# Optimization experiments

Hardware: AMD Instinct MI355X
Metric: run time of the kernel (lower is better)

The kernel has to match this reference:

```python
import jax, jax.numpy as jnp
import numpy as np

N, E, D_IN, D_H, D_OUT = 8000, 256000, 128, 128, 64
TEMP = 10.0       # config temperature.value (non-learnable)
WEIGHT = 1.0      # config weight.value (non-learnable)
LN_EPS = 1e-5


def _gcn_conv(x, W, b, src, dst, n):
    # PyG GCNConv: add self loops, sym-normalized aggregation, then bias.
    h = x @ W
    loop = jnp.arange(n)
    s = jnp.concatenate([src, loop])
    d = jnp.concatenate([dst, loop])
    deg = jnp.zeros((n,), h.dtype).at[d].add(1.0)
    dinv = jax.lax.rsqrt(jnp.maximum(deg, 1e-12))
    norm = dinv[s] * dinv[d]                       # [E+N]
    out = jax.ops.segment_sum(h[s] * norm[:, None], d, num_segments=n)
    return out + b


def _entropy_gradient(x, A, temperature, normalize):
    # E_i = 0.5 * sum_j A_ij ||x_i - x_j||^2  (dense adjacency, as in repo)
    sq = jnp.sum(x * x, axis=1)                    # [N]
    Ax = A @ x                                     # [N,d]
    deg = A.sum(axis=1)                            # [N]
    En = 0.5 * (deg * sq + A @ sq - 2.0 * jnp.sum(x * Ax, axis=1))
    if normalize:
        En = En / (jnp.max(En) + 1e-12)
    logits = -En / temperature
    P = jax.nn.softmax(logits)
    logP = jax.nn.log_softmax(logits)
    S = -jnp.sum(P * logP)
    c = P * (logP + S) / temperature               # dS/dE_k
    # dS/dx_i = c_i*(deg_i x_i - (Ax)_i) + (A^T c)_i x_i - (A^T (c*x))_i
    ATc = A.T @ c
    return (c[:, None] * (deg[:, None] * x - Ax)
            + ATc[:, None] * x - A.T @ (c[:, None] * x))


def _layer_norm(x, gamma, beta):
    mu = jnp.mean(x, axis=-1, keepdims=True)
    var = jnp.mean(jnp.square(x - mu), axis=-1, keepdims=True)
    return (x - mu) * jax.lax.rsqrt(var + LN_EPS) * gamma + beta


def setup_inputs() -> dict:
    key = jax.random.key(0)
    ks = jax.random.split(key, 6)
    def w(k, i, o):
        return jax.random.normal(k, (i, o), jnp.float32) / np.sqrt(i).astype(np.float32)
    return {
        "x": jax.random.normal(ks[0], (N, D_IN), jnp.float32),
        "edge_index": jax.random.randint(ks[1], (2, E), 0, N),
        "W1": w(ks[2], D_IN, D_H), "b1": jnp.zeros((D_H,), jnp.float32),
        "W2": w(ks[3], D_H, D_H), "b2": jnp.zeros((D_H,), jnp.float32),
        "W_out": w(ks[4], D_H, D_OUT), "b_out": jnp.zeros((D_OUT,), jnp.float32),
        "ln_gamma": jnp.ones((D_H,), jnp.float32),
        "ln_beta": jnp.zeros((D_H,), jnp.float32),
    }


def reference(x, edge_index, W1, b1, W2, b2, W_out, b_out, ln_gamma, ln_beta):
    n = x.shape[0]
    src, dst = edge_index[0], edge_index[1]
    # dense adjacency (to_dense_adj sums duplicate edges)
    A = jnp.zeros((n, n), x.dtype).at[src, dst].add(1.0)
    for W, b in ((W1, b1), (W2, b2)):
        h = _gcn_conv(x, W, b, src, dst, n)
        eg = jax.lax.stop_gradient(_entropy_gradient(h, A, TEMP, True))
        h = h + WEIGHT * eg
        h = jax.nn.relu(h)
        x = _layer_norm(h, ln_gamma, ln_beta)
    embedding = _gcn_conv(x, W_out, b_out, src, dst, n)
    return embedding
```

## Files before the change

### kernel.cpp

```cpp
#include <hip/hip_runtime.h>
#include <hip/hip_bf16.h>

#define DH 128

static constexpr float TEMP_ = 10.0f;
static constexpr float LN_EPS_ = 1e-5f;

__device__ __forceinline__ float bf2f(unsigned short u) {
  union { unsigned int i; float f; } v; v.i = ((unsigned int)u) << 16; return v.f;
}
__device__ __forceinline__ unsigned short f2bf(float f) {
  union { float f; unsigned int i; } v; v.f = f;
  unsigned int b = v.i + 0x7FFFu + ((v.i >> 16) & 1u);
  return (unsigned short)(b >> 16);
}
__device__ __forceinline__ float4 us4f4(ushort4 u) {
  return make_float4(bf2f(u.x), bf2f(u.y), bf2f(u.z), bf2f(u.w));
}
__device__ __forceinline__ ushort4 f4us4(float4 f) {
  ushort4 u; u.x = f2bf(f.x); u.y = f2bf(f.y); u.z = f2bf(f.z); u.w = f2bf(f.w);
  return u;
}

__device__ __forceinline__ float4 f4_fma(float a, float4 x, float4 y) {
  y.x = fmaf(a, x.x, y.x); y.y = fmaf(a, x.y, y.y);
  y.z = fmaf(a, x.z, y.z); y.w = fmaf(a, x.w, y.w);
  return y;
}
__device__ __forceinline__ float4 f4_add(float4 a, float4 b) {
  a.x += b.x; a.y += b.y; a.z += b.z; a.w += b.w; return a;
}
__device__ __forceinline__ float f4_hsum(float4 a) { return (a.x + a.y) + (a.z + a.w); }

__device__ __forceinline__ float grp_sum32(float v) {
  #pragma unroll
  for (int o = 16; o > 0; o >>= 1) v += __shfl_down(v, o, 32);
  return __shfl(v, 0, 32);
}

__global__ void k_hist(const int* __restrict__ ei, int E, int* cnt_d, int* cnt_s) {
  int e = blockIdx.x * blockDim.x + threadIdx.x;
  if (e < E) {
    atomicAdd(&cnt_s[ei[e]], 1);
    atomicAdd(&cnt_d[ei[E + e]], 1);
  }
}

__global__ __launch_bounds__(1024) void k_scan(int* cnt_d, int* cnt_s,
                                               int* off_d, int* off_s,
                                               float* dinv, float* dego, int n) {
  __shared__ int sm[1024];
  const int t = threadIdx.x;
  const int pass = blockIdx.x;
  int* cnt = pass ? cnt_s : cnt_d;
  int* off = pass ? off_s : off_d;
  const int base = t * 8;
  int lc[8]; int s = 0;
  #pragma unroll
  for (int j = 0; j < 8; ++j) {
    int idx = base + j;
    int v = (idx < n) ? cnt[idx] : 0;
    lc[j] = v; s += v;
  }
  sm[t] = s; __syncthreads();
  for (int o = 1; o < 1024; o <<= 1) {
    int v = (t >= o) ? sm[t - o] : 0;
    __syncthreads();
    sm[t] += v;
    __syncthreads();
  }
  int run = sm[t] - s;
  int total = sm[1023];
  #pragma unroll
  for (int j = 0; j < 8; ++j) {
    int idx = base + j;
    if (idx < n) {
      off[idx] = run; run += lc[j];
      if (pass == 0) dinv[idx] = rsqrtf((float)lc[j] + 1.0f);
      else           dego[idx] = (float)lc[j];
      cnt[idx] = 0;
    }
  }
  if (t == 0) off[n] = total;
}

__global__ void k_fill(const int* __restrict__ ei, int E,
                       const int* __restrict__ off_d, const int* __restrict__ off_s,
                       int* cnt_d, int* cnt_s, int* idx_d, int* idx_s) {
  int e = blockIdx.x * blockDim.x + threadIdx.x;
  if (e < E) {
    int s = ei[e], d = ei[E + e];
    int p = atomicAdd(&cnt_d[d], 1);
    idx_d[off_d[d] + p] = s;
    int q = atomicAdd(&cnt_s[s], 1);
    idx_s[off_s[s] + q] = d;
  }
}

template <int DOUT>
__global__ __launch_bounds__(256) void k_gemm(const float* __restrict__ X,
                                              const float* __restrict__ W,
                                              unsigned short* __restrict__ Hb) {
  __shared__ float Ws[64 * DOUT];
  __shared__ float xs[16 * 128];
  const int t = threadIdx.x;
  const int row0 = blockIdx.x * 16;

  const float4* xg = (const float4*)(X + row0 * 128);
  float4* xs4 = (float4*)xs;
  xs4[t] = xg[t];
  xs4[t + 256] = xg[t + 256];

  constexpr int RPT = (16 * DOUT) / 256;
  const int c = t % DOUT;
  const int rg = t / DOUT;
  float acc[RPT];
  #pragma unroll
  for (int r = 0; r < RPT; ++r) acc[r] = 0.f;

  for (int kt = 0; kt < 2; ++kt) {
    __syncthreads();
    for (int i = t; i < 64 * DOUT; i += 256) Ws[i] = W[kt * 64 * DOUT + i];
    __syncthreads();
    for (int k = 0; k < 64; ++k) {
      float wv = Ws[k * DOUT + c];
      #pragma unroll
      for (int r = 0; r < RPT; ++r)
        acc[r] += xs[(rg * RPT + r) * 128 + kt * 64 + k] * wv;
    }
  }
  #pragma unroll
  for (int r = 0; r < RPT; ++r)
    Hb[(row0 + rg * RPT + r) * DOUT + c] = f2bf(acc[r]);
}

__global__ __launch_bounds__(256) void k_conv_agg(const unsigned short* __restrict__ Hb,
                                                  const float* __restrict__ dinv,
                                                  const float* __restrict__ b,
                                                  const int* __restrict__ off_d,
                                                  const int* __restrict__ idx_d,
                                                  float* __restrict__ G,
                                                  unsigned short* __restrict__ Gb,
                                                  float* __restrict__ sq) {
  const int lane = threadIdx.x & 31;
  const int i = blockIdx.x * 8 + (threadIdx.x >> 5);
  const ushort4* Hv = (const ushort4*)Hb;
  const float di = dinv[i];
  float4 acc = us4f4(Hv[i * 32 + lane]);
  acc.x *= di; acc.y *= di; acc.z *= di; acc.w *= di;
  int o = off_d[i];
  const int oe = off_d[i + 1];
  for (; o + 4 <= oe; o += 4) {
    int s0 = idx_d[o], s1 = idx_d[o + 1], s2 = idx_d[o + 2], s3 = idx_d[o + 3];
    ushort4 r0 = Hv[s0 * 32 + lane], r1 = Hv[s1 * 32 + lane];
    ushort4 r2 = Hv[s2 * 32 + lane], r3 = Hv[s3 * 32 + lane];
    float d0 = dinv[s0], d1 = dinv[s1], d2 = dinv[s2], d3 = dinv[s3];
    acc = f4_fma(d0, us4f4(r0), acc); acc = f4_fma(d1, us4f4(r1), acc);
    acc = f4_fma(d2, us4f4(r2), acc); acc = f4_fma(d3, us4f4(r3), acc);
  }
  for (; o < oe; ++o) {
    int s = idx_d[o];
    acc = f4_fma(dinv[s], us4f4(Hv[s * 32 + lane]), acc);
  }
  float4 bb = ((const float4*)b)[lane];
  float4 gi;
  gi.x = fmaf(di, acc.x, bb.x); gi.y = fmaf(di, acc.y, bb.y);
  gi.z = fmaf(di, acc.z, bb.z); gi.w = fmaf(di, acc.w, bb.w);
  ((float4*)G)[i * 32 + lane] = gi;
  ((ushort4*)Gb)[i * 32 + lane] = f4us4(gi);
  float s2 = grp_sum32(gi.x * gi.x + gi.y * gi.y + gi.z * gi.z + gi.w * gi.w);
  if (lane == 0) sq[i] = s2;
}

__global__ __launch_bounds__(256) void k_ax_en(const float* __restrict__ G,
                                               const unsigned short* __restrict__ Gb,
                                               const float* __restrict__ sq,
                                               const float* __restrict__ dego,
                                               const int* __restrict__ off_s,
                                               const int* __restrict__ idx_s,
                                               float* __restrict__ Ax,
                                               float* __restrict__ En) {
  const int lane = threadIdx.x & 31;
  const int i = blockIdx.x * 8 + (threadIdx.x >> 5);
  const ushort4* Gv = (const ushort4*)Gb;
  float4 axf = make_float4(0.f, 0.f, 0.f, 0.f);
  float asq = 0.f;
  int o = off_s[i];
  const int oe = off_s[i + 1];
  for (; o + 4 <= oe; o += 4) {
    int d0 = idx_s[o], d1 = idx_s[o + 1], d2 = idx_s[o + 2], d3 = idx_s[o + 3];
    ushort4 r0 = Gv[d0 * 32 + lane], r1 = Gv[d1 * 32 + lane];
    ushort4 r2 = Gv[d2 * 32 + lane], r3 = Gv[d3 * 32 + lane];
    asq += (sq[d0] + sq[d1]) + (sq[d2] + sq[d3]);
    axf = f4_add(axf, f4_add(f4_add(us4f4(r0), us4f4(r1)),
                             f4_add(us4f4(r2), us4f4(r3))));
  }
  for (; o < oe; ++o) {
    int d = idx_s[o];
    axf = f4_add(axf, us4f4(Gv[d * 32 + lane]));
    asq += sq[d];
  }
  ((float4*)Ax)[i * 32 + lane] = axf;
  float4 gi = ((const float4*)G)[i * 32 + lane];
  float dot = grp_sum32(gi.x * axf.x + gi.y * axf.y + gi.z * axf.z + gi.w * axf.w);
  if (lane == 0) En[i] = 0.5f * (dego[i] * sq[i] + asq - 2.f * dot);
}

__device__ __forceinline__ float red1024(float v, bool domax, float* sm) {
  #pragma unroll
  for (int o = 32; o > 0; o >>= 1) {
    float u = __shfl_down(v, o, 64);
    v = domax ? fmaxf(v, u) : v + u;
  }
  if ((threadIdx.x & 63) == 0) sm[threadIdx.x >> 6] = v;
  __syncthreads();
  if (threadIdx.x == 0) {
    float r = sm[0];
    for (int k = 1; k < 16; ++k) r = domax ? fmaxf(r, sm[k]) : r + sm[k];
    sm[0] = r;
  }
  __syncthreads();
  float r = sm[0];
  __syncthreads();
  return r;
}

__global__ __launch_bounds__(1024) void k_softc(const float* __restrict__ En,
                                                float* __restrict__ c, int n) {
  __shared__ float sm[16];
  const int t = threadIdx.x;
  float m = -1e30f;
  for (int i = t; i < n; i += 1024) m = fmaxf(m, En[i]);
  m = red1024(m, true, sm);
  const float denom = (m + 1e-12f) * TEMP_;
  float se = 0.f;
  for (int i = t; i < n; i += 1024) se += expf(-En[i] / denom);
  se = red1024(se, false, sm);
  const float logZ = logf(se);
  float Sacc = 0.f;
  for (int i = t; i < n; i += 1024) {
    float li = -En[i] / denom;
    float P = expf(li) / se;
    Sacc -= P * (li - logZ);
  }
  float S = red1024(Sacc, false, sm);
  for (int i = t; i < n; i += 1024) {
    float li = -En[i] / denom;
    float P = expf(li) / se;
    c[i] = P * ((li - logZ) + S) / TEMP_;
  }
}

__global__ __launch_bounds__(256) void k_combine_ln(const float* __restrict__ G,
                                                    const unsigned short* __restrict__ Gb,
                                                    const float* __restrict__ Ax,
                                                    const float* __restrict__ cvec,
                                                    const float* __restrict__ dego,
                                                    const int* __restrict__ off_d,
                                                    const int* __restrict__ idx_d,
                                                    const float* __restrict__ gamma,
                                                    const float* __restrict__ beta,
                                                    float* __restrict__ Xout) {
  const int lane = threadIdx.x & 31;
  const int i = blockIdx.x * 8 + (threadIdx.x >> 5);
  const ushort4* Gv = (const ushort4*)Gb;
  const float4 gi = ((const float4*)G)[i * 32 + lane];
  float4 tf = make_float4(0.f, 0.f, 0.f, 0.f);
  float atc = 0.f;
  int o = off_d[i];
  const int oe = off_d[i + 1];
  for (; o + 4 <= oe; o += 4) {
    int s0 = idx_d[o], s1 = idx_d[o + 1], s2 = idx_d[o + 2], s3 = idx_d[o + 3];
    ushort4 r0 = Gv[s0 * 32 + lane], r1 = Gv[s1 * 32 + lane];
    ushort4 r2 = Gv[s2 * 32 + lane], r3 = Gv[s3 * 32 + lane];
    float c0 = cvec[s0], c1 = cvec[s1], c2 = cvec[s2], c3 = cvec[s3];
    atc += (c0 + c1) + (c2 + c3);
    tf = f4_fma(c0, us4f4(r0), tf); tf = f4_fma(c1, us4f4(r1), tf);
    tf = f4_fma(c2, us4f4(r2), tf); tf = f4_fma(c3, us4f4(r3), tf);
  }
  for (; o < oe; ++o) {
    int s = idx_d[o];
    float cs = cvec[s];
    atc += cs;
    tf = f4_fma(cs, us4f4(Gv[s * 32 + lane]), tf);
  }
  const float ci = cvec[i], dg = dego[i];
  const float4 axi = ((const float4*)Ax)[i * 32 + lane];
  float4 v;
  v.x = fmaxf(gi.x + ci * (dg * gi.x - axi.x) + atc * gi.x - tf.x, 0.f);
  v.y = fmaxf(gi.y + ci * (dg * gi.y - axi.y) + atc * gi.y - tf.y, 0.f);
  v.z = fmaxf(gi.z + ci * (dg * gi.z - axi.z) + atc * gi.z - tf.z, 0.f);
  v.w = fmaxf(gi.w + ci * (dg * gi.w - axi.w) + atc * gi.w - tf.w, 0.f);
  float mu = grp_sum32(f4_hsum(v)) * (1.f / 128.f);
  float4 dv;
  dv.x = v.x - mu; dv.y = v.y - mu; dv.z = v.z - mu; dv.w = v.w - mu;
  float var = grp_sum32(dv.x * dv.x + dv.y * dv.y + dv.z * dv.z + dv.w * dv.w) * (1.f / 128.f);
  float rs = rsqrtf(var + LN_EPS_);
  float4 ga = ((const float4*)gamma)[lane];
  float4 be = ((const float4*)beta)[lane];
  float4 out;
  out.x = fmaf(dv.x * rs, ga.x, be.x);
  out.y = fmaf(dv.y * rs, ga.y, be.y);
  out.z = fmaf(dv.z * rs, ga.z, be.z);
  out.w = fmaf(dv.w * rs, ga.w, be.w);
  ((float4*)Xout)[i * 32 + lane] = out;
}

__global__ __launch_bounds__(256) void k_final_agg(const unsigned short* __restrict__ Hb,
                                                   const float* __restrict__ dinv,
                                                   const float* __restrict__ bout,
                                                   const int* __restrict__ off_d,
                                                   const int* __restrict__ idx_d,
                                                   float* __restrict__ out) {
  const int lane = threadIdx.x & 15;
  const int i = blockIdx.x * 16 + (threadIdx.x >> 4);
  const ushort4* Hv = (const ushort4*)Hb;
  const float di = dinv[i];
  float4 acc = us4f4(Hv[i * 16 + lane]);
  acc.x *= di; acc.y *= di; acc.z *= di; acc.w *= di;
  int o = off_d[i];
  const int oe = off_d[i + 1];
  for (; o + 4 <= oe; o += 4) {
    int s0 = idx_d[o], s1 = idx_d[o + 1], s2 = idx_d[o + 2], s3 = idx_d[o + 3];
    ushort4 r0 = Hv[s0 * 16 + lane], r1 = Hv[s1 * 16 + lane];
    ushort4 r2 = Hv[s2 * 16 + lane], r3 = Hv[s3 * 16 + lane];
    acc = f4_fma(dinv[s0], us4f4(r0), acc); acc = f4_fma(dinv[s1], us4f4(r1), acc);
    acc = f4_fma(dinv[s2], us4f4(r2), acc); acc = f4_fma(dinv[s3], us4f4(r3), acc);
  }
  for (; o < oe; ++o) {
    int s = idx_d[o];
    acc = f4_fma(dinv[s], us4f4(Hv[s * 16 + lane]), acc);
  }
  float4 bb = ((const float4*)bout)[lane];
  float4 r;
  r.x = fmaf(di, acc.x, bb.x); r.y = fmaf(di, acc.y, bb.y);
  r.z = fmaf(di, acc.z, bb.z); r.w = fmaf(di, acc.w, bb.w);
  ((float4*)out)[i * 16 + lane] = r;
}

extern "C" void kernel_launch(void* const* d_in, const int* in_sizes, int n_in,
                              void* d_out, int out_size, void* d_ws, size_t ws_size,
                              hipStream_t stream) {
  const float* x    = (const float*)d_in[0];
  const int*   ei   = (const int*)d_in[1];
  const float* W1   = (const float*)d_in[2];
  const float* b1   = (const float*)d_in[3];
  const float* W2   = (const float*)d_in[4];
  const float* b2   = (const float*)d_in[5];
  const float* Wout = (const float*)d_in[6];
  const float* bout = (const float*)d_in[7];
  const float* gam  = (const float*)d_in[8];
  const float* bet  = (const float*)d_in[9];
  float* out = (float*)d_out;

  const int N = in_sizes[0] / DH;
  const int E = in_sizes[1] / 2;

  float* ws = (float*)d_ws;
  float* xf = ws;   ws += N * DH;
  float* G  = ws;   ws += N * DH;
  float* Ax = ws;   ws += N * DH;
  float* sq = ws;   ws += N;
  float* En = ws;   ws += N;
  float* cv = ws;   ws += N;
  float* dinv = ws; ws += N;
  float* dego = ws; ws += N;
  unsigned short* Hb = (unsigned short*)ws; ws += N * DH / 2;
  unsigned short* Gb = (unsigned short*)ws; ws += N * DH / 2;
  int* cnt_d = (int*)ws; ws += N;
  int* cnt_s = (int*)ws; ws += N;
  int* off_d = (int*)ws; ws += N + 4;
  int* off_s = (int*)ws; ws += N + 4;
  int* idx_d = (int*)ws; ws += E;
  int* idx_s = (int*)ws; ws += E;

  hipMemsetAsync(cnt_d, 0, 2 * N * sizeof(int), stream);
  k_hist<<<(E + 255) / 256, 256, 0, stream>>>(ei, E, cnt_d, cnt_s);
  k_scan<<<2, 1024, 0, stream>>>(cnt_d, cnt_s, off_d, off_s, dinv, dego, N);
  k_fill<<<(E + 255) / 256, 256, 0, stream>>>(ei, E, off_d, off_s, cnt_d, cnt_s,
                                              idx_d, idx_s);

  const float* xin = x;
  const float* Wl[2] = {W1, W2};
  const float* bl[2] = {b1, b2};
  for (int l = 0; l < 2; ++l) {
    k_gemm<DH><<<N / 16, 256, 0, stream>>>(xin, Wl[l], Hb);
    k_conv_agg<<<N / 8, 256, 0, stream>>>(Hb, dinv, bl[l], off_d, idx_d, G, Gb, sq);
    k_ax_en<<<N / 8, 256, 0, stream>>>(G, Gb, sq, dego, off_s, idx_s, Ax, En);
    k_softc<<<1, 1024, 0, stream>>>(En, cv, N);
    k_combine_ln<<<N / 8, 256, 0, stream>>>(G, Gb, Ax, cv, dego, off_d, idx_d,
                                            gam, bet, xf);
    xin = xf;
  }
  k_gemm<64><<<N / 16, 256, 0, stream>>>(xf, Wout, Hb);
  k_final_agg<<<N / 16, 256, 0, stream>>>(Hb, dinv, bout, off_d, idx_d, out);
}
```

Before: 277.3 us.

## Fuse softmax-entropy coefficients into combine kernel and merge histogram with first GEMM

Removes the single-block softmax/entropy kernel. Each combine_ln block now redundantly reduces the max and the exp-sums over all N energies, then recomputes the coefficient c per neighbor from En inline. The edge histogram is also folded into the first layer's GEMM launch as extra blocks, saving a launch and overlapping the atomics with the matmul. In exchange, every one of the 1000 blocks rereads the full En array and runs two block reductions, plus extra exp work per edge, and fast __expf/__logf replace the precise versions.

Measured after the change: 271.2 us. 2.2% less time.

```diff
diff --git a/kernel.cpp b/kernel.cpp
--- a/kernel.cpp
+++ b/kernel.cpp
@@ -38,12 +38,98 @@
   return __shfl(v, 0, 32);
 }
 
-__global__ void k_hist(const int* __restrict__ ei, int E, int* cnt_d, int* cnt_s) {
-  int e = blockIdx.x * blockDim.x + threadIdx.x;
-  if (e < E) {
-    atomicAdd(&cnt_s[ei[e]], 1);
-    atomicAdd(&cnt_d[ei[E + e]], 1);
-  }
+__device__ __forceinline__ float blkred(float v, bool mx, float* s4) {
+  const int t = threadIdx.x;
+  #pragma unroll
+  for (int o = 32; o > 0; o >>= 1) {
+    float u = __shfl_down(v, o, 64);
+    v = mx ? fmaxf(v, u) : v + u;
+  }
+  __syncthreads();
+  if ((t & 63) == 0) s4[t >> 6] = v;
+  __syncthreads();
+  float r = mx ? fmaxf(fmaxf(s4[0], s4[1]), fmaxf(s4[2], s4[3]))
+               : (s4[0] + s4[1]) + (s4[2] + s4[3]);
+  __syncthreads();
+  return r;
+}
+
+__global__ __launch_bounds__(256) void k_gemm1_hist(const float* __restrict__ X,
+                                                    const float* __restrict__ W,
+                                                    unsigned short* __restrict__ Hb,
+                                                    const int* __restrict__ ei, int E,
+                                                    int* cnt_d, int* cnt_s, int NT) {
+  __shared__ float Ws[64 * DH];
+  __shared__ float xs[16 * 128];
+  const int t = threadIdx.x;
+  if ((int)blockIdx.x < NT) {
+    const int row0 = blockIdx.x * 16;
+    const float4* xg = (const float4*)(X + row0 * 128);
+    float4* xs4 = (float4*)xs;
+    xs4[t] = xg[t];
+    xs4[t + 256] = xg[t + 256];
+    const int c = t & 127, rg = t >> 7;
+    float acc[8];
+    #pragma unroll
+    for (int r = 0; r < 8; ++r) acc[r] = 0.f;
+    for (int kt = 0; kt < 2; ++kt) {
+      __syncthreads();
+      for (int i = t; i < 64 * DH; i += 256) Ws[i] = W[kt * 64 * DH + i];
+      __syncthreads();
+      for (int k = 0; k < 64; ++k) {
+        float wv = Ws[k * DH + c];
+        #pragma unroll
+        for (int r = 0; r < 8; ++r)
+          acc[r] += xs[(rg * 8 + r) * 128 + kt * 64 + k] * wv;
+      }
+    }
+    #pragma unroll
+    for (int r = 0; r < 8; ++r)
+      Hb[(row0 + rg * 8 + r) * DH + c] = f2bf(acc[r]);
+  } else {
+    const int nb = gridDim.x - NT;
+    for (int e = (blockIdx.x - NT) * 256 + t; e < E; e += nb * 256) {
+      atomicAdd(&cnt_s[ei[e]], 1);
+      atomicAdd(&cnt_d[ei[E + e]], 1);
+    }
+  }
+}
+
+template <int DOUT>
+__global__ __launch_bounds__(256) void k_gemm(const float* __restrict__ X,
+                                              const float* __restrict__ W,
+                                              unsigned short* __restrict__ Hb) {
+  __shared__ float Ws[64 * DOUT];
+  __shared__ float xs[16 * 128];
+  const int t = threadIdx.x;
+  const int row0 = blockIdx.x * 16;
+
+  const float4* xg = (const float4*)(X + row0 * 128);
+  float4* xs4 = (float4*)xs;
+  xs4[t] = xg[t];
+  xs4[t + 256] = xg[t + 256];
+
+  constexpr int RPT = (16 * DOUT) / 256;
+  const int c = t % DOUT;
+  const int rg = t / DOUT;
+  float acc[RPT];
+  #pragma unroll
+  for (int r = 0; r < RPT; ++r) acc[r] = 0.f;
+
+  for (int kt = 0; kt < 2; ++kt) {
+    __syncthreads();
+    for (int i = t; i < 64 * DOUT; i += 256) Ws[i] = W[kt * 64 * DOUT + i];
+    __syncthreads();
+    for (int k = 0; k < 64; ++k) {
+      float wv = Ws[k * DOUT + c];
+      #pragma unroll
+      for (int r = 0; r < RPT; ++r)
+        acc[r] += xs[(rg * RPT + r) * 128 + kt * 64 + k] * wv;
+    }
+  }
+  #pragma unroll
+  for (int r = 0; r < RPT; ++r)
+    Hb[(row0 + rg * RPT + r) * DOUT + c] = f2bf(acc[r]);
 }
 
 __global__ __launch_bounds__(1024) void k_scan(int* cnt_d, int* cnt_s,
@@ -95,43 +181,6 @@
     int q = atomicAdd(&cnt_s[s], 1);
     idx_s[off_s[s] + q] = d;
   }
-}
-
-template <int DOUT>
-__global__ __launch_bounds__(256) void k_gemm(const float* __restrict__ X,
-                                              const float* __restrict__ W,
-                                              unsigned short* __restrict__ Hb) {
-  __shared__ float Ws[64 * DOUT];
-  __shared__ float xs[16 * 128];
-  const int t = threadIdx.x;
-  const int row0 = blockIdx.x * 16;
-
-  const float4* xg = (const float4*)(X + row0 * 128);
-  float4* xs4 = (float4*)xs;
-  xs4[t] = xg[t];
-  xs4[t + 256] = xg[t + 256];
-
-  constexpr int RPT = (16 * DOUT) / 256;
-  const int c = t % DOUT;
-  const int rg = t / DOUT;
-  float acc[RPT];
-  #pragma unroll
-  for (int r = 0; r < RPT; ++r) acc[r] = 0.f;
-
-  for (int kt = 0; kt < 2; ++kt) {
-    __syncthreads();
-    for (int i = t; i < 64 * DOUT; i += 256) Ws[i] = W[kt * 64 * DOUT + i];
-    __syncthreads();
-    for (int k = 0; k < 64; ++k) {
-      float wv = Ws[k * DOUT + c];
-      #pragma unroll
-      for (int r = 0; r < RPT; ++r)
-        acc[r] += xs[(rg * RPT + r) * 128 + kt * 64 + k] * wv;
-    }
-  }
-  #pragma unroll
-  for (int r = 0; r < RPT; ++r)
-    Hb[(row0 + rg * RPT + r) * DOUT + c] = f2bf(acc[r]);
 }
 
 __global__ __launch_bounds__(256) void k_conv_agg(const unsigned short* __restrict__ Hb,
@@ -206,63 +255,37 @@
   if (lane == 0) En[i] = 0.5f * (dego[i] * sq[i] + asq - 2.f * dot);
 }
 
-__device__ __forceinline__ float red1024(float v, bool domax, float* sm) {
-  #pragma unroll
-  for (int o = 32; o > 0; o >>= 1) {
-    float u = __shfl_down(v, o, 64);
-    v = domax ? fmaxf(v, u) : v + u;
-  }
-  if ((threadIdx.x & 63) == 0) sm[threadIdx.x >> 6] = v;
-  __syncthreads();
-  if (threadIdx.x == 0) {
-    float r = sm[0];
-    for (int k = 1; k < 16; ++k) r = domax ? fmaxf(r, sm[k]) : r + sm[k];
-    sm[0] = r;
-  }
-  __syncthreads();
-  float r = sm[0];
-  __syncthreads();
-  return r;
-}
-
-__global__ __launch_bounds__(1024) void k_softc(const float* __restrict__ En,
-                                                float* __restrict__ c, int n) {
-  __shared__ float sm[16];
-  const int t = threadIdx.x;
-  float m = -1e30f;
-  for (int i = t; i < n; i += 1024) m = fmaxf(m, En[i]);
-  m = red1024(m, true, sm);
-  const float denom = (m + 1e-12f) * TEMP_;
-  float se = 0.f;
-  for (int i = t; i < n; i += 1024) se += expf(-En[i] / denom);
-  se = red1024(se, false, sm);
-  const float logZ = logf(se);
-  float Sacc = 0.f;
-  for (int i = t; i < n; i += 1024) {
-    float li = -En[i] / denom;
-    float P = expf(li) / se;
-    Sacc -= P * (li - logZ);
-  }
-  float S = red1024(Sacc, false, sm);
-  for (int i = t; i < n; i += 1024) {
-    float li = -En[i] / denom;
-    float P = expf(li) / se;
-    c[i] = P * ((li - logZ) + S) / TEMP_;
-  }
-}
-
 __global__ __launch_bounds__(256) void k_combine_ln(const float* __restrict__ G,
                                                     const unsigned short* __restrict__ Gb,
                                                     const float* __restrict__ Ax,
-                                                    const float* __restrict__ cvec,
+                                                    const float* __restrict__ En,
                                                     const float* __restrict__ dego,
                                                     const int* __restrict__ off_d,
                                                     const int* __restrict__ idx_d,
                                                     const float* __restrict__ gamma,
                                                     const float* __restrict__ beta,
-                                                    float* __restrict__ Xout) {
-  const int lane = threadIdx.x & 31;
-  const int i = blockIdx.x * 8 + (threadIdx.x >> 5);
+                                                    float* __restrict__ Xout, int n) {
+  __shared__ float s4[4];
+  const int t = threadIdx.x;
+  float mloc = -3.0e38f;
+  for (int k = t; k < n; k += 256) mloc = fmaxf(mloc, En[k]);
+  const float m = blkred(mloc, true, s4);
+  const float invden = -1.0f / ((m + 1e-12f) * TEMP_);
+  float se = 0.f, sl = 0.f;
+  for (int k = t; k < n; k += 256) {
+    float li = En[k] * invden;
+    float e = __expf(li);
+    se += e; sl += e * li;
+  }
+  se = blkred(se, false, s4);
+  sl = blkred(sl, false, s4);
+  const float logZ = __logf(se);
+  const float S = logZ - sl / se;
+  const float cmul = (1.0f / se) * (1.0f / TEMP_);
+  const float cadd = S - logZ;
+
+  const int lane = t & 31;
+  const int i = blockIdx.x * 8 + (t >> 5);
   const ushort4* Gv = (const ushort4*)Gb;
   const float4 gi = ((const float4*)G)[i * 32 + lane];
   float4 tf = make_float4(0.f, 0.f, 0.f, 0.f);
@@ -273,18 +296,26 @@
     int s0 = idx_d[o], s1 = idx_d[o + 1], s2 = idx_d[o + 2], s3 = idx_d[o + 3];
     ushort4 r0 = Gv[s0 * 32 + lane], r1 = Gv[s1 * 32 + lane];
     ushort4 r2 = Gv[s2 * 32 + lane], r3 = Gv[s3 * 32 + lane];
-    float c0 = cvec[s0], c1 = cvec[s1], c2 = cvec[s2], c3 = cvec[s3];
+    float l0 = En[s0] * invden, l1 = En[s1] * invden;
+    float l2 = En[s2] * invden, l3 = En[s3] * invden;
+    float c0 = __expf(l0) * cmul * (l0 + cadd);
+    float c1 = __expf(l1) * cmul * (l1 + cadd);
+    float c2 = __expf(l2) * cmul * (l2 + cadd);
+    float c3 = __expf(l3) * cmul * (l3 + cadd);
     atc += (c0 + c1) + (c2 + c3);
     tf = f4_fma(c0, us4f4(r0), tf); tf = f4_fma(c1, us4f4(r1), tf);
     tf = f4_fma(c2, us4f4(r2), tf); tf = f4_fma(c3, us4f4(r3), tf);
   }
   for (; o < oe; ++o) {
     int s = idx_d[o];
-    float cs = cvec[s];
+    float ls = En[s] * invden;
+    float cs = __expf(ls) * cmul * (ls + cadd);
     atc += cs;
     tf = f4_fma(cs, us4f4(Gv[s * 32 + lane]), tf);
   }
-  const float ci = cvec[i], dg = dego[i];
+  const float li_i = En[i] * invden;
+  const float ci = __expf(li_i) * cmul * (li_i + cadd);
+  const float dg = dego[i];
   const float4 axi = ((const float4*)Ax)[i * 32 + lane];
   float4 v;
   v.x = fmaxf(gi.x + ci * (dg * gi.x - axi.x) + atc * gi.x - tf.x, 0.f);
@@ -362,7 +393,6 @@
   float* Ax = ws;   ws += N * DH;
   float* sq = ws;   ws += N;
   float* En = ws;   ws += N;
-  float* cv = ws;   ws += N;
   float* dinv = ws; ws += N;
   float* dego = ws; ws += N;
   unsigned short* Hb = (unsigned short*)ws; ws += N * DH / 2;
@@ -374,23 +404,21 @@
   int* idx_d = (int*)ws; ws += E;
   int* idx_s = (int*)ws; ws += E;
 
+  const int NT = N / 16;
+
   hipMemsetAsync(cnt_d, 0, 2 * N * sizeof(int), stream);
-  k_hist<<<(E + 255) / 256, 256, 0, stream>>>(ei, E, cnt_d, cnt_s);
+  k_gemm1_hist<<<NT + 256, 256, 0, stream>>>(x, W1, Hb, ei, E, cnt_d, cnt_s, NT);
   k_scan<<<2, 1024, 0, stream>>>(cnt_d, cnt_s, off_d, off_s, dinv, dego, N);
   k_fill<<<(E + 255) / 256, 256, 0, stream>>>(ei, E, off_d, off_s, cnt_d, cnt_s,
                                               idx_d, idx_s);
 
-  const float* xin = x;
-  const float* Wl[2] = {W1, W2};
-  const float* bl[2] = {b1, b2};
   for (int l = 0; l < 2; ++l) {
-    k_gemm<DH><<<N / 16, 256, 0, stream>>>(xin, Wl[l], Hb);
-    k_conv_agg<<<N / 8, 256, 0, stream>>>(Hb, dinv, bl[l], off_d, idx_d, G, Gb, sq);
+    if (l) k_gemm<DH><<<N / 16, 256, 0, stream>>>(xf, W2, Hb);
+    k_conv_agg<<<N / 8, 256, 0, stream>>>(Hb, dinv, l ? b2 : b1, off_d, idx_d,
+                                          G, Gb, sq);
     k_ax_en<<<N / 8, 256, 0, stream>>>(G, Gb, sq, dego, off_s, idx_s, Ax, En);
-    k_softc<<<1, 1024, 0, stream>>>(En, cv, N);
-    k_combine_ln<<<N / 8, 256, 0, stream>>>(G, Gb, Ax, cv, dego, off_d, idx_d,
-                                            gam, bet, xf);
-    xin = xf;
+    k_combine_ln<<<N / 8, 256, 0, stream>>>(G, Gb, Ax, En, dego, off_d, idx_d,
+                                            gam, bet, xf, N);
   }
   k_gemm<64><<<N / 16, 256, 0, stream>>>(xf, Wout, Hb);
   k_final_agg<<<N / 16, 256, 0, stream>>>(Hb, dinv, bout, off_d, idx_d, out);
```
